# Kernel optimization log

Measured on AMD Instinct MI355X. Metric: run time of the kernel, lower is better.

Reference implementation:

```python
import jax, jax.numpy as jnp
import numpy as np

N_NODES = 20000
N_EDGES = 320000
IN_CH = 256
HID_CH = 256   # 2 * out_channels
OUT_CH = 128


def gcn_conv(x, edge_index, W, b, n_nodes):
    """PyG GCNConv: linear transform, add self-loops, sym-normalized scatter-add."""
    x = x @ W  # [N, C_out]
    loop = jnp.arange(n_nodes, dtype=edge_index.dtype)
    row = jnp.concatenate([edge_index[0], loop])  # source nodes
    col = jnp.concatenate([edge_index[1], loop])  # destination nodes
    deg = jax.ops.segment_sum(jnp.ones_like(col, dtype=x.dtype), col,
                              num_segments=n_nodes)
    deg_inv_sqrt = jnp.where(deg > 0, jax.lax.rsqrt(deg), 0.0)
    norm = deg_inv_sqrt[row] * deg_inv_sqrt[col]  # [E+N]
    msg = x[row] * norm[:, None]                  # gather + scale
    out = jax.ops.segment_sum(msg, col, num_segments=n_nodes)  # scatter-add
    return out + b


def setup_inputs() -> dict:
    key = jax.random.key(0)
    k1, k2, k3, k4, k5 = jax.random.split(key, 5)
    doc_embeds = jax.random.normal(k1, (N_NODES, IN_CH), dtype=jnp.float32)
    edge_index = jax.random.randint(k2, (2, N_EDGES), 0, N_NODES, dtype=jnp.int64)
    # Glorot-style init for GCN weights, zero bias (PyG defaults)
    s1 = 1.0 / np.sqrt(IN_CH)
    s2 = 1.0 / np.sqrt(HID_CH)
    W1 = jax.random.uniform(k3, (IN_CH, HID_CH), jnp.float32, -s1, s1)
    b1 = jnp.zeros((HID_CH,), jnp.float32)
    W2 = jax.random.uniform(k4, (HID_CH, OUT_CH), jnp.float32, -s2, s2)
    b2 = jnp.zeros((OUT_CH,), jnp.float32)
    return {"doc_embeds": doc_embeds, "edge_index": edge_index,
            "W1": W1, "b1": b1, "W2": W2, "b2": b2}


def reference(doc_embeds, edge_index, W1, b1, W2, b2):
    n = doc_embeds.shape[0]
    x = jax.nn.relu(gcn_conv(doc_embeds, edge_index, W1, b1, n))
    x = gcn_conv(x, edge_index, W2, b2, n)
    return x
```

## Files before the change

kernel.cpp:

```cpp
#include <hip/hip_runtime.h>
#include <math.h>

#define N_NODES 20000
#define N_EDGES 320000
#define IN_CH   256
#define HID_CH  256
#define OUT_CH  128
#define CAP     64

typedef __attribute__((ext_vector_type(8))) short short8;
typedef __attribute__((ext_vector_type(8))) unsigned short ushort8;
typedef __attribute__((ext_vector_type(4))) unsigned short ushort4v;
typedef __attribute__((ext_vector_type(4))) float floatx4;
typedef __attribute__((ext_vector_type(4))) _Float16 half4;

static __device__ __forceinline__ unsigned short f2bf(float f) {
    unsigned int u = __float_as_uint(f);
    u += 0x7FFFu + ((u >> 16) & 1u);
    return (unsigned short)(u >> 16);
}
static __device__ __forceinline__ float bf2f(unsigned short h) {
    return __uint_as_float(((unsigned int)h) << 16);
}

__global__ __launch_bounds__(256)
void init_kernel(const float* __restrict__ W1, const float* __restrict__ W2,
                 unsigned short* __restrict__ W1thi, unsigned short* __restrict__ W1tlo,
                 unsigned short* __restrict__ W2thi, unsigned short* __restrict__ W2tlo,
                 int* __restrict__ deg) {
    const int g = blockIdx.x * blockDim.x + threadIdx.x;
    const int gsz = gridDim.x * blockDim.x;
    for (int i = g; i < N_NODES; i += gsz) deg[i] = 0;
    for (int t = g; t < (IN_CH * HID_CH) / 16; t += gsz) {
        int n = t >> 4;
        int kc = (t & 15) * 16;
        ushort8 h0, l0, h1, l1;
#pragma unroll
        for (int j = 0; j < 8; ++j) {
            float x = W1[(size_t)(kc + j) * HID_CH + n];
            h0[j] = f2bf(x); l0[j] = f2bf(x - bf2f(h0[j]));
            float y = W1[(size_t)(kc + 8 + j) * HID_CH + n];
            h1[j] = f2bf(y); l1[j] = f2bf(y - bf2f(h1[j]));
        }
        *(ushort8*)(W1thi + (size_t)n * IN_CH + kc)     = h0;
        *(ushort8*)(W1thi + (size_t)n * IN_CH + kc + 8) = h1;
        *(ushort8*)(W1tlo + (size_t)n * IN_CH + kc)     = l0;
        *(ushort8*)(W1tlo + (size_t)n * IN_CH + kc + 8) = l1;
    }
    for (int t = g; t < (HID_CH * OUT_CH) / 16; t += gsz) {
        int n = t >> 4;
        int kc = (t & 15) * 16;
        ushort8 h0, l0, h1, l1;
#pragma unroll
        for (int j = 0; j < 8; ++j) {
            float x = W2[(size_t)(kc + j) * OUT_CH + n];
            h0[j] = f2bf(x); l0[j] = f2bf(x - bf2f(h0[j]));
            float y = W2[(size_t)(kc + 8 + j) * OUT_CH + n];
            h1[j] = f2bf(y); l1[j] = f2bf(y - bf2f(h1[j]));
        }
        *(ushort8*)(W2thi + (size_t)n * HID_CH + kc)     = h0;
        *(ushort8*)(W2thi + (size_t)n * HID_CH + kc + 8) = h1;
        *(ushort8*)(W2tlo + (size_t)n * HID_CH + kc)     = l0;
        *(ushort8*)(W2tlo + (size_t)n * HID_CH + kc + 8) = l1;
    }
}

__global__ void degfill_kernel(const int* __restrict__ row, const int* __restrict__ col,
                               int* __restrict__ deg, unsigned short* __restrict__ srcs, int E) {
    int i = blockIdx.x * blockDim.x + threadIdx.x;
    if (i < E) {
        int c = col[i];
        int r = row[i];
        int p = atomicAdd(&deg[c], 1);
        srcs[(size_t)c * CAP + p] = (unsigned short)r;
    }
}

#define GK 256
template <int AFP32, int TM>
__global__ __launch_bounds__(256)
void gemm_mfma_kernel(const float* __restrict__ Afp,
                      const unsigned short* __restrict__ Ahi, const unsigned short* __restrict__ Alo,
                      const unsigned short* __restrict__ Bthi, const unsigned short* __restrict__ Btlo,
                      const int* __restrict__ deg, _Float16* __restrict__ C, int M, int N) {
    constexpr int MI = TM / 32;
    __shared__ unsigned short As[2][TM][36];
    __shared__ unsigned short Bs[2][128][36];
    const int tid = threadIdx.x;
    const int m0 = blockIdx.y * TM;
    const int n0 = blockIdx.x * 128;
    const int lane = tid & 63;
    const int wave = tid >> 6;
    const int wr = (wave >> 1) * (TM / 2);
    const int wc = (wave & 1) * 64;
    const int lm = lane & 15;
    const int lk = (lane >> 4) * 8;

    floatx4 acc[MI][4];
#pragma unroll
    for (int i = 0; i < MI; ++i)
#pragma unroll
        for (int j = 0; j < 4; ++j) acc[i][j] = (floatx4){0.f, 0.f, 0.f, 0.f};

    for (int k0 = 0; k0 < GK; k0 += 32) {
#pragma unroll
        for (int c = 0; c < TM / 64; ++c) {
            int ch = tid + c * 256;
            int r = ch >> 2;
            int ko = (ch & 3) * 8;
            ushort8 vh = {}, vl = {};
            if (m0 + r < M) {
                if (AFP32) {
                    const float* ap = Afp + (size_t)(m0 + r) * GK + k0 + ko;
                    float4 f0 = *(const float4*)ap;
                    float4 f1 = *(const float4*)(ap + 4);
                    float xs[8] = {f0.x, f0.y, f0.z, f0.w, f1.x, f1.y, f1.z, f1.w};
#pragma unroll
                    for (int j = 0; j < 8; ++j) {
                        vh[j] = f2bf(xs[j]);
                        vl[j] = f2bf(xs[j] - bf2f(vh[j]));
                    }
                } else {
                    size_t ga = (size_t)(m0 + r) * GK + k0 + ko;
                    vh = *(const ushort8*)(Ahi + ga);
                    vl = *(const ushort8*)(Alo + ga);
                }
            }
            *(ushort8*)&As[0][r][ko] = vh;
            *(ushort8*)&As[1][r][ko] = vl;
        }
#pragma unroll
        for (int c = 0; c < 2; ++c) {
            int ch = tid + c * 256;
            int r = ch >> 2;
            int ko = (ch & 3) * 8;
            size_t gb = (size_t)(n0 + r) * GK + k0 + ko;
            *(ushort8*)&Bs[0][r][ko] = *(const ushort8*)(Bthi + gb);
            *(ushort8*)&Bs[1][r][ko] = *(const ushort8*)(Btlo + gb);
        }
        __syncthreads();

        short8 ah[MI], al[MI], bh[4], bl[4];
#pragma unroll
        for (int i = 0; i < MI; ++i) {
            ah[i] = *(const short8*)&As[0][wr + i * 16 + lm][lk];
            al[i] = *(const short8*)&As[1][wr + i * 16 + lm][lk];
        }
#pragma unroll
        for (int j = 0; j < 4; ++j) {
            bh[j] = *(const short8*)&Bs[0][wc + j * 16 + lm][lk];
            bl[j] = *(const short8*)&Bs[1][wc + j * 16 + lm][lk];
        }
#pragma unroll
        for (int i = 0; i < MI; ++i)
#pragma unroll
            for (int j = 0; j < 4; ++j) {
                acc[i][j] = __builtin_amdgcn_mfma_f32_16x16x32_bf16(ah[i], bh[j], acc[i][j], 0, 0, 0);
                acc[i][j] = __builtin_amdgcn_mfma_f32_16x16x32_bf16(ah[i], bl[j], acc[i][j], 0, 0, 0);
                acc[i][j] = __builtin_amdgcn_mfma_f32_16x16x32_bf16(al[i], bh[j], acc[i][j], 0, 0, 0);
            }
        __syncthreads();
    }

#pragma unroll
    for (int i = 0; i < MI; ++i) {
#pragma unroll
        for (int r = 0; r < 4; ++r) {
            int rowi = m0 + wr + i * 16 + (lane >> 4) * 4 + r;
            if (rowi < M) {
                float dr = 1.0f / sqrtf((float)(deg[rowi] + 1));
#pragma unroll
                for (int j = 0; j < 4; ++j) {
                    C[(size_t)rowi * N + n0 + wc + j * 16 + lm] = (_Float16)(dr * acc[i][j][r]);
                }
            }
        }
    }
}

template <int C, int NSLICE, int MODE>
__global__ __launch_bounds__(256)
void gather_sliced_kernel(const _Float16* __restrict__ X, const int* __restrict__ deg,
                          const unsigned short* __restrict__ srcs,
                          const float* __restrict__ bias, float* __restrict__ outf,
                          unsigned short* __restrict__ outhi, unsigned short* __restrict__ outlo,
                          int n) {
    constexpr int SW = C / NSLICE;
    static_assert(SW == 32, "slice must be 32 channels");
    const int slice = blockIdx.x % NSLICE;
    const int ngrp  = blockIdx.x / NSLICE;
    const int wave = threadIdx.x >> 6;
    const int lane = threadIdx.x & 63;
    const int g  = lane >> 3;
    const int sl = lane & 7;
    const int node = ngrp * 32 + wave * 8 + g;
    if (node >= n) return;
    const int choff = slice * SW + sl * 4;
    const size_t beg = (size_t)node * CAP;
    const int cnt = deg[node];

    float4 acc = make_float4(0.f, 0.f, 0.f, 0.f);
    int e = 0;
    for (; e + 4 <= cnt; e += 4) {
        ushort4v s4 = *(const ushort4v*)(srcs + beg + e);
        half4 v0 = *(const half4*)(X + (size_t)s4.x * C + choff);
        half4 v1 = *(const half4*)(X + (size_t)s4.y * C + choff);
        half4 v2 = *(const half4*)(X + (size_t)s4.z * C + choff);
        half4 v3 = *(const half4*)(X + (size_t)s4.w * C + choff);
        acc.x += (float)v0.x + (float)v1.x + (float)v2.x + (float)v3.x;
        acc.y += (float)v0.y + (float)v1.y + (float)v2.y + (float)v3.y;
        acc.z += (float)v0.z + (float)v1.z + (float)v2.z + (float)v3.z;
        acc.w += (float)v0.w + (float)v1.w + (float)v2.w + (float)v3.w;
    }
    for (; e < cnt; ++e) {
        int r = srcs[beg + e];
        half4 v = *(const half4*)(X + (size_t)r * C + choff);
        acc.x += (float)v.x; acc.y += (float)v.y;
        acc.z += (float)v.z; acc.w += (float)v.w;
    }

    const float dc = 1.0f / sqrtf((float)(cnt + 1));
    half4 vsh = *(const half4*)(X + (size_t)node * C + choff);
    float4 bb = *(const float4*)(bias + choff);

    float o0 = dc * (acc.x + (float)vsh.x) + bb.x;
    float o1 = dc * (acc.y + (float)vsh.y) + bb.y;
    float o2 = dc * (acc.z + (float)vsh.z) + bb.z;
    float o3 = dc * (acc.w + (float)vsh.w) + bb.w;

    if constexpr (MODE == 1) {
        o0 = fmaxf(o0, 0.f); o1 = fmaxf(o1, 0.f);
        o2 = fmaxf(o2, 0.f); o3 = fmaxf(o3, 0.f);
        ushort4v h, l;
        h.x = f2bf(o0); l.x = f2bf(o0 - bf2f(h.x));
        h.y = f2bf(o1); l.y = f2bf(o1 - bf2f(h.y));
        h.z = f2bf(o2); l.z = f2bf(o2 - bf2f(h.z));
        h.w = f2bf(o3); l.w = f2bf(o3 - bf2f(h.w));
        *(ushort4v*)(outhi + (size_t)node * C + choff) = h;
        *(ushort4v*)(outlo + (size_t)node * C + choff) = l;
    } else {
        floatx4 o = {o0, o1, o2, o3};
        __builtin_nontemporal_store(o, (floatx4*)(outf + (size_t)node * C + choff));
    }
}

extern "C" void kernel_launch(void* const* d_in, const int* in_sizes, int n_in,
                              void* d_out, int out_size, void* d_ws, size_t ws_size,
                              hipStream_t stream) {
    const float* doc_embeds = (const float*)d_in[0];
    const int*   edge_index = (const int*)d_in[1];
    const float* W1 = (const float*)d_in[2];
    const float* b1 = (const float*)d_in[3];
    const float* W2 = (const float*)d_in[4];
    const float* b2 = (const float*)d_in[5];
    float* out = (float*)d_out;

    const int* row = edge_index;
    const int* col = edge_index + N_EDGES;

    char* ws = (char*)d_ws;
    auto align_up = [](size_t x) { return (x + 255) / 256 * 256; };

    _Float16*       X1s  = (_Float16*)(ws);
    unsigned short* H1hi = (unsigned short*)(ws + align_up((size_t)N_NODES * HID_CH * 2));
    unsigned short* H1lo = H1hi + (size_t)N_NODES * HID_CH;
    _Float16*       X2s  = X1s;
    char* meta = (char*)(H1lo + (size_t)N_NODES * HID_CH);
    unsigned short* W1thi = (unsigned short*)(meta); meta += align_up((size_t)IN_CH * HID_CH * 2);
    unsigned short* W1tlo = (unsigned short*)(meta); meta += align_up((size_t)IN_CH * HID_CH * 2);
    unsigned short* W2thi = (unsigned short*)(meta); meta += align_up((size_t)HID_CH * OUT_CH * 2);
    unsigned short* W2tlo = (unsigned short*)(meta); meta += align_up((size_t)HID_CH * OUT_CH * 2);
    int*            deg   = (int*)(meta);            meta += align_up((size_t)N_NODES * 4);
    unsigned short* srcs  = (unsigned short*)(meta);

    init_kernel<<<256, 256, 0, stream>>>(W1, W2, W1thi, W1tlo, W2thi, W2tlo, deg);
    degfill_kernel<<<(N_EDGES + 255) / 256, 256, 0, stream>>>(row, col, deg, srcs, N_EDGES);

    {
        dim3 grid(HID_CH / 128, (N_NODES + 63) / 64);
        gemm_mfma_kernel<1, 64><<<grid, 256, 0, stream>>>(
            doc_embeds, nullptr, nullptr, W1thi, W1tlo, deg, X1s, N_NODES, HID_CH);
    }
    gather_sliced_kernel<HID_CH, 8, 1><<<((N_NODES + 31) / 32) * 8, 256, 0, stream>>>(
        X1s, deg, srcs, b1, nullptr, H1hi, H1lo, N_NODES);

    {
        dim3 grid(OUT_CH / 128, (N_NODES + 63) / 64);
        gemm_mfma_kernel<0, 64><<<grid, 256, 0, stream>>>(
            nullptr, H1hi, H1lo, W2thi, W2tlo, deg, X2s, N_NODES, OUT_CH);
    }
    gather_sliced_kernel<OUT_CH, 4, 0><<<((N_NODES + 31) / 32) * 4, 256, 0, stream>>>(
        X2s, deg, srcs, b2, out, nullptr, nullptr, N_NODES);
}
```

Baseline: 177.7 us.

## Fuse layer-1 aggregation with ReLU into the layer-2 GEMM A-tile load

```diff
diff --git a/kernel.cpp b/kernel.cpp
--- a/kernel.cpp
+++ b/kernel.cpp
@@ -77,53 +77,42 @@
 }
 
 #define GK 256
-template <int AFP32, int TM>
 __global__ __launch_bounds__(256)
-void gemm_mfma_kernel(const float* __restrict__ Afp,
-                      const unsigned short* __restrict__ Ahi, const unsigned short* __restrict__ Alo,
-                      const unsigned short* __restrict__ Bthi, const unsigned short* __restrict__ Btlo,
-                      const int* __restrict__ deg, _Float16* __restrict__ C, int M, int N) {
-    constexpr int MI = TM / 32;
-    __shared__ unsigned short As[2][TM][36];
+void gemm1_kernel(const float* __restrict__ Afp,
+                  const unsigned short* __restrict__ Bthi, const unsigned short* __restrict__ Btlo,
+                  const int* __restrict__ deg, _Float16* __restrict__ C, int M, int N) {
+    __shared__ unsigned short As[2][64][36];
     __shared__ unsigned short Bs[2][128][36];
     const int tid = threadIdx.x;
-    const int m0 = blockIdx.y * TM;
+    const int m0 = blockIdx.y * 64;
     const int n0 = blockIdx.x * 128;
     const int lane = tid & 63;
     const int wave = tid >> 6;
-    const int wr = (wave >> 1) * (TM / 2);
+    const int wr = (wave >> 1) * 32;
     const int wc = (wave & 1) * 64;
     const int lm = lane & 15;
     const int lk = (lane >> 4) * 8;
 
-    floatx4 acc[MI][4];
-#pragma unroll
-    for (int i = 0; i < MI; ++i)
+    floatx4 acc[2][4];
+#pragma unroll
+    for (int i = 0; i < 2; ++i)
 #pragma unroll
         for (int j = 0; j < 4; ++j) acc[i][j] = (floatx4){0.f, 0.f, 0.f, 0.f};
 
     for (int k0 = 0; k0 < GK; k0 += 32) {
-#pragma unroll
-        for (int c = 0; c < TM / 64; ++c) {
-            int ch = tid + c * 256;
-            int r = ch >> 2;
-            int ko = (ch & 3) * 8;
+        {
+            int r = tid >> 2;
+            int ko = (tid & 3) * 8;
             ushort8 vh = {}, vl = {};
             if (m0 + r < M) {
-                if (AFP32) {
-                    const float* ap = Afp + (size_t)(m0 + r) * GK + k0 + ko;
-                    float4 f0 = *(const float4*)ap;
-                    float4 f1 = *(const float4*)(ap + 4);
-                    float xs[8] = {f0.x, f0.y, f0.z, f0.w, f1.x, f1.y, f1.z, f1.w};
-#pragma unroll
-                    for (int j = 0; j < 8; ++j) {
-                        vh[j] = f2bf(xs[j]);
-                        vl[j] = f2bf(xs[j] - bf2f(vh[j]));
-                    }
-                } else {
-                    size_t ga = (size_t)(m0 + r) * GK + k0 + ko;
-                    vh = *(const ushort8*)(Ahi + ga);
-                    vl = *(const ushort8*)(Alo + ga);
+                const float* ap = Afp + (size_t)(m0 + r) * GK + k0 + ko;
+                float4 f0 = *(const float4*)ap;
+                float4 f1 = *(const float4*)(ap + 4);
+                float xs[8] = {f0.x, f0.y, f0.z, f0.w, f1.x, f1.y, f1.z, f1.w};
+#pragma unroll
+                for (int j = 0; j < 8; ++j) {
+                    vh[j] = f2bf(xs[j]);
+                    vl[j] = f2bf(xs[j] - bf2f(vh[j]));
                 }
             }
             *(ushort8*)&As[0][r][ko] = vh;
@@ -140,9 +129,9 @@
         }
         __syncthreads();
 
-        short8 ah[MI], al[MI], bh[4], bl[4];
-#pragma unroll
-        for (int i = 0; i < MI; ++i) {
+        short8 ah[2], al[2], bh[4], bl[4];
+#pragma unroll
+        for (int i = 0; i < 2; ++i) {
             ah[i] = *(const short8*)&As[0][wr + i * 16 + lm][lk];
             al[i] = *(const short8*)&As[1][wr + i * 16 + lm][lk];
         }
@@ -152,7 +141,7 @@
             bl[j] = *(const short8*)&Bs[1][wc + j * 16 + lm][lk];
         }
 #pragma unroll
-        for (int i = 0; i < MI; ++i)
+        for (int i = 0; i < 2; ++i)
 #pragma unroll
             for (int j = 0; j < 4; ++j) {
                 acc[i][j] = __builtin_amdgcn_mfma_f32_16x16x32_bf16(ah[i], bh[j], acc[i][j], 0, 0, 0);
@@ -163,7 +152,7 @@
     }
 
 #pragma unroll
-    for (int i = 0; i < MI; ++i) {
+    for (int i = 0; i < 2; ++i) {
 #pragma unroll
         for (int r = 0; r < 4; ++r) {
             int rowi = m0 + wr + i * 16 + (lane >> 4) * 4 + r;
@@ -178,13 +167,117 @@
     }
 }
 
-template <int C, int NSLICE, int MODE>
+__global__ __launch_bounds__(256)
+void gemm2_fused_kernel(const _Float16* __restrict__ X1, const int* __restrict__ deg,
+                        const unsigned short* __restrict__ srcs, const float* __restrict__ b1,
+                        const unsigned short* __restrict__ Bthi, const unsigned short* __restrict__ Btlo,
+                        _Float16* __restrict__ C, int M, int N) {
+    __shared__ unsigned short As[2][32][36];
+    __shared__ unsigned short Bs[2][128][36];
+    const int tid = threadIdx.x;
+    const int m0 = blockIdx.x * 32;
+    const int lane = tid & 63;
+    const int wave = tid >> 6;
+    const int wr = (wave >> 1) * 16;
+    const int wc = (wave & 1) * 64;
+    const int lm = lane & 15;
+    const int lk = (lane >> 4) * 8;
+
+    const int ar  = tid >> 3;
+    const int ako = (tid & 7) * 4;
+    const int m = m0 + ar;
+    const int cnt  = (m < M) ? deg[m] : 0;
+    const float dc = 1.0f / sqrtf((float)(cnt + 1));
+    const size_t sbeg = (size_t)m * CAP;
+
+    floatx4 acc[4];
+#pragma unroll
+    for (int j = 0; j < 4; ++j) acc[j] = (floatx4){0.f, 0.f, 0.f, 0.f};
+
+    for (int k0 = 0; k0 < GK; k0 += 32) {
+        {
+            ushort4v vh = {}, vl = {};
+            if (m < M) {
+                const int kc = k0 + ako;
+                float a0 = 0.f, a1 = 0.f, a2 = 0.f, a3 = 0.f;
+                int e = 0;
+                for (; e + 4 <= cnt; e += 4) {
+                    ushort4v s4 = *(const ushort4v*)(srcs + sbeg + e);
+                    half4 v0 = *(const half4*)(X1 + (size_t)s4.x * GK + kc);
+                    half4 v1 = *(const half4*)(X1 + (size_t)s4.y * GK + kc);
+                    half4 v2 = *(const half4*)(X1 + (size_t)s4.z * GK + kc);
+                    half4 v3 = *(const half4*)(X1 + (size_t)s4.w * GK + kc);
+                    a0 += (float)v0.x + (float)v1.x + (float)v2.x + (float)v3.x;
+                    a1 += (float)v0.y + (float)v1.y + (float)v2.y + (float)v3.y;
+                    a2 += (float)v0.z + (float)v1.z + (float)v2.z + (float)v3.z;
+                    a3 += (float)v0.w + (float)v1.w + (float)v2.w + (float)v3.w;
+                }
+                for (; e < cnt; ++e) {
+                    int r = srcs[sbeg + e];
+                    half4 v = *(const half4*)(X1 + (size_t)r * GK + kc);
+                    a0 += (float)v.x; a1 += (float)v.y;
+                    a2 += (float)v.z; a3 += (float)v.w;
+                }
+                half4 self = *(const half4*)(X1 + (size_t)m * GK + kc);
+                float4 bb = *(const float4*)(b1 + kc);
+                float h0 = fmaxf(dc * (a0 + (float)self.x) + bb.x, 0.f);
+                float h1 = fmaxf(dc * (a1 + (float)self.y) + bb.y, 0.f);
+                float h2 = fmaxf(dc * (a2 + (float)self.z) + bb.z, 0.f);
+                float h3 = fmaxf(dc * (a3 + (float)self.w) + bb.w, 0.f);
+                vh.x = f2bf(h0); vl.x = f2bf(h0 - bf2f(vh.x));
+                vh.y = f2bf(h1); vl.y = f2bf(h1 - bf2f(vh.y));
+                vh.z = f2bf(h2); vl.z = f2bf(h2 - bf2f(vh.z));
+                vh.w = f2bf(h3); vl.w = f2bf(h3 - bf2f(vh.w));
+            }
+            *(ushort4v*)&As[0][ar][ako] = vh;
+            *(ushort4v*)&As[1][ar][ako] = vl;
+        }
+#pragma unroll
+        for (int c = 0; c < 2; ++c) {
+            int ch = tid + c * 256;
+            int r = ch >> 2;
+            int ko = (ch & 3) * 8;
+            size_t gb = (size_t)r * GK + k0 + ko;
+            *(ushort8*)&Bs[0][r][ko] = *(const ushort8*)(Bthi + gb);
+            *(ushort8*)&Bs[1][r][ko] = *(const ushort8*)(Btlo + gb);
+        }
+        __syncthreads();
+
+        short8 ah, al, bh[4], bl[4];
+        ah = *(const short8*)&As[0][wr + lm][lk];
+        al = *(const short8*)&As[1][wr + lm][lk];
+#pragma unroll
+        for (int j = 0; j < 4; ++j) {
+            bh[j] = *(const short8*)&Bs[0][wc + j * 16 + lm][lk];
+            bl[j] = *(const short8*)&Bs[1][wc + j * 16 + lm][lk];
+        }
+#pragma unroll
+        for (int j = 0; j < 4; ++j) {
+            acc[j] = __builtin_amdgcn_mfma_f32_16x16x32_bf16(ah, bh[j], acc[j], 0, 0, 0);
+            acc[j] = __builtin_amdgcn_mfma_f32_16x16x32_bf16(ah, bl[j], acc[j], 0, 0, 0);
+            acc[j] = __builtin_amdgcn_mfma_f32_16x16x32_bf16(al, bh[j], acc[j], 0, 0, 0);
+        }
+        __syncthreads();
+    }
+
+#pragma unroll
+    for (int r = 0; r < 4; ++r) {
+        int rowi = m0 + wr + (lane >> 4) * 4 + r;
+        if (rowi < M) {
+            float dr = 1.0f / sqrtf((float)(deg[rowi] + 1));
+#pragma unroll
+            for (int j = 0; j < 4; ++j) {
+                C[(size_t)rowi * N + wc + j * 16 + lm] = (_Float16)(dr * acc[j][r]);
+            }
+        }
+    }
+}
+
+template <int C, int NSLICE>
 __global__ __launch_bounds__(256)
 void gather_sliced_kernel(const _Float16* __restrict__ X, const int* __restrict__ deg,
                           const unsigned short* __restrict__ srcs,
-                          const float* __restrict__ bias, float* __restrict__ outf,
-                          unsigned short* __restrict__ outhi, unsigned short* __restrict__ outlo,
-                          int n) {
+                          const float* __restrict__ bias, float* __restrict__ outf, int n) {
     constexpr int SW = C / NSLICE;
     static_assert(SW == 32, "slice must be 32 channels");
     const int slice = blockIdx.x % NSLICE;
@@ -223,25 +316,12 @@
     half4 vsh = *(const half4*)(X + (size_t)node * C + choff);
     float4 bb = *(const float4*)(bias + choff);
 
-    float o0 = dc * (acc.x + (float)vsh.x) + bb.x;
-    float o1 = dc * (acc.y + (float)vsh.y) + bb.y;
-    float o2 = dc * (acc.z + (float)vsh.z) + bb.z;
-    float o3 = dc * (acc.w + (float)vsh.w) + bb.w;
-
-    if constexpr (MODE == 1) {
-        o0 = fmaxf(o0, 0.f); o1 = fmaxf(o1, 0.f);
-        o2 = fmaxf(o2, 0.f); o3 = fmaxf(o3, 0.f);
-        ushort4v h, l;
-        h.x = f2bf(o0); l.x = f2bf(o0 - bf2f(h.x));
-        h.y = f2bf(o1); l.y = f2bf(o1 - bf2f(h.y));
-        h.z = f2bf(o2); l.z = f2bf(o2 - bf2f(h.z));
-        h.w = f2bf(o3); l.w = f2bf(o3 - bf2f(h.w));
-        *(ushort4v*)(outhi + (size_t)node * C + choff) = h;
-        *(ushort4v*)(outlo + (size_t)node * C + choff) = l;
-    } else {
-        floatx4 o = {o0, o1, o2, o3};
-        __builtin_nontemporal_store(o, (floatx4*)(outf + (size_t)node * C + choff));
-    }
+    floatx4 o;
+    o.x = dc * (acc.x + (float)vsh.x) + bb.x;
+    o.y = dc * (acc.y + (float)vsh.y) + bb.y;
+    o.z = dc * (acc.z + (float)vsh.z) + bb.z;
+    o.w = dc * (acc.w + (float)vsh.w) + bb.w;
+    __builtin_nontemporal_store(o, (floatx4*)(outf + (size_t)node * C + choff));
 }
 
 extern "C" void kernel_launch(void* const* d_in, const int* in_sizes, int n_in,
@@ -261,11 +341,10 @@
     char* ws = (char*)d_ws;
     auto align_up = [](size_t x) { return (x + 255) / 256 * 256; };
 
-    _Float16*       X1s  = (_Float16*)(ws);
-    unsigned short* H1hi = (unsigned short*)(ws + align_up((size_t)N_NODES * HID_CH * 2));
-    unsigned short* H1lo = H1hi + (size_t)N_NODES * HID_CH;
-    _Float16*       X2s  = X1s;
-    char* meta = (char*)(H1lo + (size_t)N_NODES * HID_CH);
+    _Float16* X1s = (_Float16*)(ws);
+    _Float16* X2s = (_Float16*)(ws + align_up((size_t)N_NODES * HID_CH * 2));
+    char* meta = (char*)(ws + align_up((size_t)N_NODES * HID_CH * 2)
+                            + align_up((size_t)N_NODES * OUT_CH * 2));
     unsigned short* W1thi = (unsigned short*)(meta); meta += align_up((size_t)IN_CH * HID_CH * 2);
     unsigned short* W1tlo = (unsigned short*)(meta); meta += align_up((size_t)IN_CH * HID_CH * 2);
     unsigned short* W2thi = (unsigned short*)(meta); meta += align_up((size_t)HID_CH * OUT_CH * 2);
@@ -278,17 +357,12 @@
 
     {
         dim3 grid(HID_CH / 128, (N_NODES + 63) / 64);
-        gemm_mfma_kernel<1, 64><<<grid, 256, 0, stream>>>(
-            doc_embeds, nullptr, nullptr, W1thi, W1tlo, deg, X1s, N_NODES, HID_CH);
-    }
-    gather_sliced_kernel<HID_CH, 8, 1><<<((N_NODES + 31) / 32) * 8, 256, 0, stream>>>(
-        X1s, deg, srcs, b1, nullptr, H1hi, H1lo, N_NODES);
-
-    {
-        dim3 grid(OUT_CH / 128, (N_NODES + 63) / 64);
-        gemm_mfma_kernel<0, 64><<<grid, 256, 0, stream>>>(
-            nullptr, H1hi, H1lo, W2thi, W2tlo, deg, X2s, N_NODES, OUT_CH);
-    }
-    gather_sliced_kernel<OUT_CH, 4, 0><<<((N_NODES + 31) / 32) * 4, 256, 0, stream>>>(
-        X2s, deg, srcs, b2, out, nullptr, nullptr, N_NODES);
-}
+        gemm1_kernel<<<grid, 256, 0, stream>>>(doc_embeds, W1thi, W1tlo, deg, X1s, N_NODES, HID_CH);
+    }
+
+    gemm2_fused_kernel<<<(N_NODES + 31) / 32, 256, 0, stream>>>(
+        X1s, deg, srcs, b1, W2thi, W2tlo, X2s, N_NODES, OUT_CH);
+
+    gather_sliced_kernel<OUT_CH, 4><<<((N_NODES + 31) / 32) * 4, 256, 0, stream>>>(
+        X2s, deg, srcs, b2, out, N_NODES);
+}
```

Result: slower. 187.6 us (+5.6%).
